# Optimization experiments

Hardware: AMD Instinct MI355X
Metric: run time of the kernel (lower is better)

The kernel has to match this reference:

```python
import jax, jax.numpy as jnp
import numpy as np

TOKENS = 8192
IN_F = 4096
OUT_F = 16384
QMAX = 256  # uint8-style affine range [0, 255]


def setup_inputs() -> dict:
    key = jax.random.key(0)
    kx, kw, kb = jax.random.split(key, 3)
    x = jax.random.normal(kx, (TOKENS, IN_F), dtype=jnp.float32)
    weight_q = jax.random.randint(kw, (OUT_F, IN_F), 0, QMAX, dtype=jnp.int32)
    bias = jax.random.normal(kb, (OUT_F,), dtype=jnp.float32)
    scale = jnp.float32(0.01)   # per-tensor affine scale
    zero_point = 128            # per-tensor affine zero point (int constant)
    return {"x": x, "weight_q": weight_q, "bias": bias, "scale": scale, "zero_point": zero_point}


def reference(x, weight_q, bias, scale, zero_point):
    # Dequantize weight: (q - zero_point) -> fp32, then dense matmul.
    # out[t, o] = (sum_i x[t, i] * (wq[o, i] - zp)) * scale + bias[o]
    w_deq = (weight_q - zero_point).astype(jnp.float32)  # [out, in]
    acc = jnp.einsum('ti,oi->to', x, w_deq)              # [tokens, out]
    return acc * scale + bias
```

## Files before the change

### kernel.cpp

```cpp
#include <hip/hip_runtime.h>
#include <hip/hip_bf16.h>
#include <stdint.h>

#define M_DIM 8192
#define N_DIM 16384
#define K_DIM 4096

typedef short short8 __attribute__((ext_vector_type(8)));
typedef float floatx4 __attribute__((ext_vector_type(4)));
typedef int i32x4 __attribute__((ext_vector_type(4)));

__device__ __forceinline__ unsigned short f2bf(float f) {
    union { float f; unsigned u; } a;
    a.f = f;
    unsigned r = a.u + 0x7FFFu + ((a.u >> 16) & 1u);
    return (unsigned short)(r >> 16);
}

#define GLDS16(g, l)                                                     \
    __builtin_amdgcn_global_load_lds(                                    \
        (const __attribute__((address_space(1))) void*)(g),              \
        (__attribute__((address_space(3))) void*)(l), 16, 0, 0)

#define SBAR() asm volatile("s_barrier" ::: "memory")
#define WAIT_LGKM0() asm volatile("s_waitcnt lgkmcnt(0)" ::: "memory")
#define WAIT_LGKM4() asm volatile("s_waitcnt lgkmcnt(4)" ::: "memory")
#define WAIT_LGKM8() asm volatile("s_waitcnt lgkmcnt(8)" ::: "memory")
#define WAIT_VM6() asm volatile("s_waitcnt vmcnt(6)" ::: "memory")
#define WAIT_VM0() asm volatile("s_waitcnt vmcnt(0)" ::: "memory")
#define SCHEDB() __builtin_amdgcn_sched_barrier(0)

__global__ __launch_bounds__(256)
void quant_x_kernel(const float4* __restrict__ x, int* __restrict__ xq,
                    float* __restrict__ sx) {
    const int row = blockIdx.x;
    const int t = threadIdx.x;
    const float4* px = x + (size_t)row * (K_DIM / 4);
    float4 v[4];
    float am = 0.f;
#pragma unroll
    for (int j = 0; j < 4; ++j) {
        v[j] = px[t + j * 256];
        am = fmaxf(am, fmaxf(fmaxf(fabsf(v[j].x), fabsf(v[j].y)),
                             fmaxf(fabsf(v[j].z), fabsf(v[j].w))));
    }
#pragma unroll
    for (int m = 32; m; m >>= 1) am = fmaxf(am, __shfl_xor(am, m));
    __shared__ float red[4];
    if ((t & 63) == 0) red[t >> 6] = am;
    __syncthreads();
    am = fmaxf(fmaxf(red[0], red[1]), fmaxf(red[2], red[3]));
    const float inv = am > 0.f ? 127.f / am : 0.f;
    if (t == 0) sx[row] = am * (1.f / 127.f);
    int* xo = xq + (size_t)row * (K_DIM / 4);
#pragma unroll
    for (int j = 0; j < 4; ++j) {
        int q0 = (int)rintf(v[j].x * inv);
        int q1 = (int)rintf(v[j].y * inv);
        int q2 = (int)rintf(v[j].z * inv);
        int q3 = (int)rintf(v[j].w * inv);
        xo[t + j * 256] = (q0 & 255) | ((q1 & 255) << 8) |
                          ((q2 & 255) << 16) | ((q3 & 255) << 24);
    }
}

__global__ void cvt_w8_kernel(const int4* __restrict__ w, int4* __restrict__ out,
                              const int* __restrict__ zp_p, int n16) {
    const int zp = *zp_p;
    int idx = blockIdx.x * blockDim.x + threadIdx.x;
    int stride = gridDim.x * blockDim.x;
    for (int i = idx; i < n16; i += stride) {
        int4 r;
        int* rp = (int*)&r;
#pragma unroll
        for (int j = 0; j < 4; ++j) {
            int4 q = w[i * 4 + j];
            rp[j] = ((q.x - zp) & 255) | (((q.y - zp) & 255) << 8) |
                    (((q.z - zp) & 255) << 16) | (((q.w - zp) & 255) << 24);
        }
        out[i] = r;
    }
}


#define LOAD_AR(BUF, MH, AF)                                               \
    do {                                                                   \
        const char* p_ = smem + (BUF)*65536 + (MH)*16384 + wm*8192;        \
        _Pragma("unroll") for (int mf = 0; mf < 4; ++mf) {                 \
            AF[mf][0] = *(const i32x4*)(p_ + mf*2048 + laneK0);            \
            AF[mf][1] = *(const i32x4*)(p_ + mf*2048 + laneK1);            \
        }                                                                  \
    } while (0)

#define LOAD_BR(BUF, NH, BF)                                               \
    do {                                                                   \
        const char* p_ = smem + (BUF)*65536 + 32768 + (NH)*16384 + wn*4096;\
        _Pragma("unroll") for (int nf = 0; nf < 2; ++nf) {                 \
            BF[nf][0] = *(const i32x4*)(p_ + nf*2048 + laneK0);            \
            BF[nf][1] = *(const i32x4*)(p_ + nf*2048 + laneK1);            \
        }                                                                  \
    } while (0)

#define STAGE_A0(BUF)                                                      \
    do {                                                                   \
        GLDS16(pA00, smem + (BUF)*65536 + st16); pA00 += 128;              \
        GLDS16(pA01, smem + (BUF)*65536 + 8192 + st16); pA01 += 128;       \
    } while (0)
#define STAGE_A1(BUF)                                                      \
    do {                                                                   \
        GLDS16(pA10, smem + (BUF)*65536 + 16384 + st16); pA10 += 128;      \
        GLDS16(pA11, smem + (BUF)*65536 + 16384 + 8192 + st16); pA11 += 128;\
    } while (0)
#define STAGE_B0(BUF)                                                      \
    do {                                                                   \
        GLDS16(pB00, smem + (BUF)*65536 + 32768 + st16); pB00 += 128;      \
        GLDS16(pB01, smem + (BUF)*65536 + 32768 + 8192 + st16); pB01 += 128;\
    } while (0)
#define STAGE_B1(BUF)                                                      \
    do {                                                                   \
        GLDS16(pB10, smem + (BUF)*65536 + 49152 + st16); pB10 += 128;      \
        GLDS16(pB11, smem + (BUF)*65536 + 49152 + 8192 + st16); pB11 += 128;\
    } while (0)

#define MFMA_Q(AF, BF, MH, NH)                                             \
    do {                                                                   \
        __builtin_amdgcn_s_setprio(1);                                     \
        _Pragma("unroll") for (int kk = 0; kk < 2; ++kk)                   \
        _Pragma("unroll") for (int mf = 0; mf < 4; ++mf)                   \
        _Pragma("unroll") for (int nf = 0; nf < 2; ++nf)                   \
            acc[(MH)*4+mf][(NH)*2+nf] =                                    \
                __builtin_amdgcn_mfma_i32_16x16x64_i8(                     \
                    AF[mf][kk], BF[nf][kk], acc[(MH)*4+mf][(NH)*2+nf],     \
                    0, 0, 0);                                              \
        __builtin_amdgcn_s_setprio(0);                                     \
    } while (0)

#define BODY(B, NB, SMODE)                                                 \
    do {                                                                   \
                       \
        LOAD_AR(B, 0, aFa);                                                \
        LOAD_BR(B, 0, bF0);                                                \
        LOAD_BR(B, 1, bF1);                                                \
        if ((SMODE) >= 1) STAGE_B0(NB);                                    \
        SBAR(); WAIT_LGKM4();                                              \
        MFMA_Q(aFa, bF0, 0, 0);                                            \
        SBAR();                                                            \
                                        \
        LOAD_AR(B, 1, aFb);                                                \
        if ((SMODE) >= 2) STAGE_A0(B);                                     \
        SBAR(); WAIT_LGKM8();                                              \
        MFMA_Q(aFa, bF1, 0, 1);                                            \
        SBAR();                                                            \
                                            \
        if ((SMODE) >= 2) STAGE_B1(B);                                     \
        SBAR(); WAIT_LGKM0();                                              \
        MFMA_Q(aFb, bF1, 1, 1);                                            \
        SBAR();                                                            \
                                \
        if ((SMODE) >= 2) STAGE_A1(B);                                     \
        SCHEDB();                                                          \
        MFMA_Q(aFb, bF0, 1, 0);                                            \
        SCHEDB();                                                          \
        if ((SMODE) == 2) { WAIT_VM6(); } else { WAIT_VM0(); }             \
        SBAR();                                                            \
    } while (0)

__global__ __launch_bounds__(512, 2)
void gemm8i_kernel(const int8_t* __restrict__ Aq, const int8_t* __restrict__ Bq,
                   const float* __restrict__ bias,
                   const float* __restrict__ scale_p,
                   const float* __restrict__ sx,
                   float* __restrict__ out) {
    __shared__ __align__(16) char smem[131072];

    const int t = threadIdx.x;
    const int lane = t & 63;
    const int wid = t >> 6;
    const int wm = wid >> 2;
    const int wn = wid & 3;

    int bid = blockIdx.x;
    int sz = (bid & 7) * 256 + (bid >> 3);
    const int bx = sz & 63;
    const int by = sz >> 6;
    const int brow = by << 8;
    const int bcol = bx << 8;

    const int laneK0 = (lane & 15) * 128 + (((lane >> 4) * 16) ^ ((lane & 7) << 4));
    const int laneK1 = (lane & 15) * 128 + ((((lane >> 4) * 16) + 64) ^ ((lane & 7) << 4));

    size_t aoffs[2], boffs[2];
#pragma unroll
    for (int g = 0; g < 2; ++g) {
        unsigned u = g * 8192 + t * 16;
        unsigned up = u ^ (((u >> 7) & 7) << 4);
        aoffs[g] = (size_t)(brow + ((up >> 13) & 1) * 128 + ((up >> 7) & 63)) * K_DIM
                   + (up & 127);
        boffs[g] = (size_t)(bcol + ((up >> 12) & 3) * 64 + ((up >> 7) & 31)) * K_DIM
                   + (up & 127);
    }
    const int8_t* pA00 = Aq + aoffs[0];
    const int8_t* pA01 = Aq + aoffs[1];
    const int8_t* pA10 = Aq + aoffs[0] + 262144;
    const int8_t* pA11 = Aq + aoffs[1] + 262144;
    const int8_t* pB00 = Bq + boffs[0];
    const int8_t* pB01 = Bq + boffs[1];
    const int8_t* pB10 = Bq + boffs[0] + 131072;
    const int8_t* pB11 = Bq + boffs[1] + 131072;
    const int st16 = t * 16;

    i32x4 acc[8][4] = {};
    i32x4 aFa[4][2], aFb[4][2], bF0[2][2], bF1[2][2];

    const int NT = K_DIM / 128;

    STAGE_A0(0);
    STAGE_B0(0);
    STAGE_B1(0);
    STAGE_A1(0);
    STAGE_A0(1);
    STAGE_B1(1);
    STAGE_A1(1);
    WAIT_VM6();
    SBAR();

    for (int it = 0; it < (NT - 2) / 2; ++it) {
        BODY(0, 1, 2);
        BODY(1, 0, 2);
    }
    BODY(0, 1, 1);
    BODY(1, 0, 0);

    const float scale = *scale_p;
    const int crow0 = brow + wm * 128 + ((lane >> 4) << 2);
    const int ccol0 = bcol + wn * 64 + (lane & 15);
    float bv[4];
#pragma unroll
    for (int nf = 0; nf < 4; ++nf) bv[nf] = bias[ccol0 + nf * 16];
#pragma unroll
    for (int mf = 0; mf < 8; ++mf) {
#pragma unroll
        for (int j = 0; j < 4; ++j) {
            const int r = crow0 + mf * 16 + j;
            const float s2 = scale * sx[r];
            float* orow = out + (size_t)r * N_DIM;
#pragma unroll
            for (int nf = 0; nf < 4; ++nf)
                orow[ccol0 + nf * 16] = (float)acc[mf][nf][j] * s2 + bv[nf];
        }
    }
}

__global__ __launch_bounds__(256)
void gemm_fb_kernel(const float* __restrict__ Xf, const int* __restrict__ Wq,
                    const float* __restrict__ bias,
                    const float* __restrict__ scale_p,
                    const int* __restrict__ zp_p,
                    float* __restrict__ out) {
    const int NB = N_DIM / 128;
    int nwg = gridDim.x;
    int cpx = nwg >> 3;
    int bid = blockIdx.x;
    int swz = (bid & 7) * cpx + (bid >> 3);
    int bx = swz % NB;
    int by = swz / NB;
    const int brow = by * 128;
    const int bcol = bx * 128;

    __shared__ __align__(16) ushort sA[128 * 32];
    __shared__ __align__(16) ushort sB[128 * 32];

    const int t = threadIdx.x;
    const int lane = t & 63;
    const int wid = t >> 6;
    const int wr = wid >> 1;
    const int wc = wid & 1;

    floatx4 acc[4][4] = {};

    const int xr = t >> 1;
    const int xc = (t & 1) << 4;
    const int zp = *zp_p;

    const int arow = wr * 64 + (lane & 15);
    const int acol = (lane >> 4) << 3;
    const int brow_f = wc * 64 + (lane & 15);

    for (int k0 = 0; k0 < K_DIM; k0 += 32) {
        __syncthreads();
        const float* gx = Xf + (size_t)(brow + xr) * K_DIM + k0 + xc;
        ushort* dA = &sA[xr * 32 + xc];
#pragma unroll
        for (int i = 0; i < 4; ++i) {
            float4 v = ((const float4*)gx)[i];
            ushort4 u;
            u.x = f2bf(v.x); u.y = f2bf(v.y); u.z = f2bf(v.z); u.w = f2bf(v.w);
            *(ushort4*)(dA + i * 4) = u;
        }
        const int* gw = Wq + (size_t)(bcol + xr) * K_DIM + k0 + xc;
        ushort* dB = &sB[xr * 32 + xc];
#pragma unroll
        for (int i = 0; i < 4; ++i) {
            int4 q = ((const int4*)gw)[i];
            ushort4 u;
            u.x = f2bf((float)(q.x - zp));
            u.y = f2bf((float)(q.y - zp));
            u.z = f2bf((float)(q.z - zp));
            u.w = f2bf((float)(q.w - zp));
            *(ushort4*)(dB + i * 4) = u;
        }
        __syncthreads();

        short8 af[4], bfr[4];
#pragma unroll
        for (int m = 0; m < 4; ++m)
            af[m] = *(const short8*)&sA[(arow + m * 16) * 32 + acol];
#pragma unroll
        for (int n = 0; n < 4; ++n)
            bfr[n] = *(const short8*)&sB[(brow_f + n * 16) * 32 + acol];

#pragma unroll
        for (int m = 0; m < 4; ++m)
#pragma unroll
            for (int n = 0; n < 4; ++n)
                acc[m][n] = __builtin_amdgcn_mfma_f32_16x16x32_bf16(
                    af[m], bfr[n], acc[m][n], 0, 0, 0);
    }

    const float scale = *scale_p;
    const int colbase = bcol + wc * 64 + (lane & 15);
    const int rowbase = brow + wr * 64 + ((lane >> 4) << 2);
    float bv[4];
#pragma unroll
    for (int n = 0; n < 4; ++n) bv[n] = bias[colbase + n * 16];
#pragma unroll
    for (int m = 0; m < 4; ++m) {
        const int r0 = rowbase + m * 16;
#pragma unroll
        for (int j = 0; j < 4; ++j) {
            float* orow = out + (size_t)(r0 + j) * N_DIM;
#pragma unroll
            for (int n = 0; n < 4; ++n)
                orow[colbase + n * 16] = acc[m][n][j] * scale + bv[n];
        }
    }
}

extern "C" void kernel_launch(void* const* d_in, const int* in_sizes, int n_in,
                              void* d_out, int out_size, void* d_ws, size_t ws_size,
                              hipStream_t stream) {
    const float* x = (const float*)d_in[0];
    const int* wq = (const int*)d_in[1];
    const float* bias = (const float*)d_in[2];
    const float* scale = (const float*)d_in[3];
    const int* zp = (const int*)d_in[4];
    float* out = (float*)d_out;

    const size_t xq_bytes = (size_t)M_DIM * K_DIM;
    const size_t wb_bytes = (size_t)N_DIM * K_DIM;
    const size_t sx_bytes = (size_t)M_DIM * 4;

    if (ws_size >= xq_bytes + wb_bytes + sx_bytes) {
        int8_t* xq = (int8_t*)d_ws;
        int8_t* wb = (int8_t*)d_ws + xq_bytes;
        float* sx = (float*)((char*)d_ws + xq_bytes + wb_bytes);
        quant_x_kernel<<<M_DIM, 256, 0, stream>>>((const float4*)x, (int*)xq, sx);
        cvt_w8_kernel<<<2048, 256, 0, stream>>>((const int4*)wq, (int4*)wb, zp,
                                                (N_DIM * K_DIM) / 16);
        const int nblocks = (M_DIM / 256) * (N_DIM / 256);
        gemm8i_kernel<<<nblocks, 512, 0, stream>>>(xq, wb, bias, scale, sx, out);
    } else {
        const int nblocks = (M_DIM / 128) * (N_DIM / 128);
        gemm_fb_kernel<<<nblocks, 256, 0, stream>>>(x, wq, bias, scale, zp, out);
    }
}
```

Measured before the change: 733.7 us.

## Restructure int8 GEMM main loop to prefetch next-tile fragments across iterations

Reworks the double-buffered main loop so the next tile's A and B0 register fragments are loaded from LDS during the last MFMA quarter of the current tile, using ping-pong bF0 registers. All four stage loads for the next tile are now issued together, and the lgkmcnt waits plus sched barriers are replaced with finer vmcnt waits. The aim is to hide LDS read latency behind MFMAs and drop one barrier-separated wait per phase. The cost is higher register pressure from the extra fragment buffer, plus a risk that the changed wait counts or staging order cause races.

```diff
diff --git a/kernel.cpp b/kernel.cpp
--- a/kernel.cpp
+++ b/kernel.cpp
@@ -23,12 +23,11 @@
         (__attribute__((address_space(3))) void*)(l), 16, 0, 0)
 
 #define SBAR() asm volatile("s_barrier" ::: "memory")
-#define WAIT_LGKM0() asm volatile("s_waitcnt lgkmcnt(0)" ::: "memory")
-#define WAIT_LGKM4() asm volatile("s_waitcnt lgkmcnt(4)" ::: "memory")
-#define WAIT_LGKM8() asm volatile("s_waitcnt lgkmcnt(8)" ::: "memory")
-#define WAIT_VM6() asm volatile("s_waitcnt vmcnt(6)" ::: "memory")
 #define WAIT_VM0() asm volatile("s_waitcnt vmcnt(0)" ::: "memory")
-#define SCHEDB() __builtin_amdgcn_sched_barrier(0)
+#define WAIT_VM2() asm volatile("s_waitcnt vmcnt(2)" ::: "memory")
+#define WAIT_VM4() asm volatile("s_waitcnt vmcnt(4)" ::: "memory")
+#define WAIT_VM8() asm volatile("s_waitcnt vmcnt(8)" ::: "memory")
+#define WAIT_VM10() asm volatile("s_waitcnt vmcnt(10)" ::: "memory")
 
 __global__ __launch_bounds__(256)
 void quant_x_kernel(const float4* __restrict__ x, int* __restrict__ xq,
@@ -135,33 +134,30 @@
         __builtin_amdgcn_s_setprio(0);                                     \
     } while (0)
 
-#define BODY(B, NB, SMODE)                                                 \
-    do {                                                                   \
-                       \
-        LOAD_AR(B, 0, aFa);                                                \
-        LOAD_BR(B, 0, bF0);                                                \
+#define BODY(B, NB, SMODE, BF0C, BF0N)                                     \
+    do {                                                                   \
+                                             \
         LOAD_BR(B, 1, bF1);                                                \
-        if ((SMODE) >= 1) STAGE_B0(NB);                                    \
-        SBAR(); WAIT_LGKM4();                                              \
-        MFMA_Q(aFa, bF0, 0, 0);                                            \
+        MFMA_Q(aFa, BF0C, 0, 0);                                           \
+        if ((SMODE) == 0) { WAIT_VM0(); } else { WAIT_VM8(); }             \
         SBAR();                                                            \
-                                        \
+                         \
         LOAD_AR(B, 1, aFb);                                                \
-        if ((SMODE) >= 2) STAGE_A0(B);                                     \
-        SBAR(); WAIT_LGKM8();                                              \
+        if ((SMODE) == 2) { STAGE_A0(B); STAGE_B0(B); }                    \
         MFMA_Q(aFa, bF1, 0, 1);                                            \
         SBAR();                                                            \
-                                            \
-        if ((SMODE) >= 2) STAGE_B1(B);                                     \
-        SBAR(); WAIT_LGKM0();                                              \
+                                         \
+        if ((SMODE) == 2) STAGE_B1(B);                                     \
         MFMA_Q(aFb, bF1, 1, 1);                                            \
+        if ((SMODE) == 2) { WAIT_VM10(); }                                 \
+        else if ((SMODE) == 1) { WAIT_VM4(); }                             \
         SBAR();                                                            \
-                                \
-        if ((SMODE) >= 2) STAGE_A1(B);                                     \
-        SCHEDB();                                                          \
-        MFMA_Q(aFb, bF0, 1, 0);                                            \
-        SCHEDB();                                                          \
-        if ((SMODE) == 2) { WAIT_VM6(); } else { WAIT_VM0(); }             \
+            \
+        if ((SMODE) >= 1) { LOAD_AR(NB, 0, aFa); LOAD_BR(NB, 0, BF0N); }   \
+        if ((SMODE) == 2) STAGE_A1(B);                                     \
+        MFMA_Q(aFb, BF0C, 1, 0);                                           \
+        if ((SMODE) == 2) { WAIT_VM10(); }                                 \
+        else if ((SMODE) == 1) { WAIT_VM2(); }                             \
         SBAR();                                                            \
     } while (0)
 
@@ -210,26 +206,23 @@
     const int st16 = t * 16;
 
     i32x4 acc[8][4] = {};
-    i32x4 aFa[4][2], aFb[4][2], bF0[2][2], bF1[2][2];
+    i32x4 aFa[4][2], aFb[4][2], bF0A[2][2], bF0B[2][2], bF1[2][2];
 
     const int NT = K_DIM / 128;
 
-    STAGE_A0(0);
-    STAGE_B0(0);
-    STAGE_B1(0);
-    STAGE_A1(0);
-    STAGE_A0(1);
-    STAGE_B1(1);
-    STAGE_A1(1);
-    WAIT_VM6();
+    STAGE_A0(0); STAGE_B0(0); STAGE_B1(0); STAGE_A1(0);
+    STAGE_A0(1); STAGE_B0(1); STAGE_B1(1); STAGE_A1(1);
+    WAIT_VM8();
     SBAR();
+    LOAD_AR(0, 0, aFa);
+    LOAD_BR(0, 0, bF0A);
 
     for (int it = 0; it < (NT - 2) / 2; ++it) {
-        BODY(0, 1, 2);
-        BODY(1, 0, 2);
-    }
-    BODY(0, 1, 1);
-    BODY(1, 0, 0);
+        BODY(0, 1, 2, bF0A, bF0B);
+        BODY(1, 0, 2, bF0B, bF0A);
+    }
+    BODY(0, 1, 1, bF0A, bF0B);
+    BODY(1, 0, 0, bF0B, bF0A);
 
     const float scale = *scale_p;
     const int crow0 = brow + wm * 128 + ((lane >> 4) << 2);
```

Result: slower. 1.286 ms (+75.2%).
